# Optimization experiments

Hardware: AMD Instinct MI355X
Metric: run time of the kernel (lower is better)

The kernel has to match this reference:

```python
import jax, jax.numpy as jnp
import numpy as np

N_NODES = 100000
N_EDGES = 1600000
D_IN = 16
D_HID = 32   # 2 * out_channels
D_OUT = 16


def gcn_conv(h, src, dst, W, b, num_nodes):
    """PyG-style GCNConv: x' = D^{-1/2} (A+I) D^{-1/2} (x W) + b.
    src/dst already include self-loops."""
    h = h @ W                                   # [N, F_out] linear transform first
    deg = jnp.zeros((num_nodes,), h.dtype).at[dst].add(1.0)
    dinv = jax.lax.rsqrt(jnp.maximum(deg, 1.0))  # deg >= 1 due to self-loops
    norm = dinv[src] * dinv[dst]                # [E+N]
    msg = h[src] * norm[:, None]                # edge gather (memory-bound)
    out = jax.ops.segment_sum(msg, dst, num_segments=num_nodes)
    return out + b


def setup_inputs() -> dict:
    key = jax.random.key(0)
    k1, k2, k3, k4 = jax.random.split(key, 4)
    x = jnp.arange(N_NODES, dtype=jnp.int32)
    edge_index = jax.random.randint(k1, (2, N_EDGES), 0, N_NODES, dtype=jnp.int32)
    emb = jax.random.normal(k2, (N_NODES, D_IN), dtype=jnp.float32)
    W1 = jax.random.normal(k3, (D_IN, D_HID), dtype=jnp.float32) * (1.0 / np.sqrt(D_IN))
    b1 = jnp.zeros((D_HID,), jnp.float32)
    W2 = jax.random.normal(k4, (D_HID, D_OUT), dtype=jnp.float32) * (1.0 / np.sqrt(D_HID))
    b2 = jnp.zeros((D_OUT,), jnp.float32)
    return {"x": x, "edge_index": edge_index, "emb": emb,
            "W1": W1, "b1": b1, "W2": W2, "b2": b2}


def reference(x, edge_index, emb, W1, b1, W2, b2):
    num_nodes = emb.shape[0]
    # add self-loops once; reused by both conv layers
    loops = jnp.arange(num_nodes, dtype=edge_index.dtype)
    src = jnp.concatenate([edge_index[0], loops])
    dst = jnp.concatenate([edge_index[1], loops])

    h = emb[x]                                  # embedding lookup
    h = jax.nn.relu(gcn_conv(h, src, dst, W1, b1, num_nodes))
    # dropout is identity in eval mode (reference baseline)
    out = gcn_conv(h, src, dst, W2, b2, num_nodes)
    return out
```

## Files before the change

kernel.cpp:

```cpp
#include <hip/hip_runtime.h>


#define BS   256
#define BSBIG 1024
#define NBLK 256
#define BINSHIFT 8
#define BIN  256
#define MAXBINS 512
#define BINCAP 4608

union H2 { int i; _Float16 h[2]; };

__global__ __launch_bounds__(BSBIG) void k_hist(
    const int* __restrict__ dst, int E, int NBINS, int* __restrict__ histG) {
    __shared__ int h[MAXBINS];
    int t = threadIdx.x;
    for (int i = t; i < NBINS; i += BSBIG) h[i] = 0;
    __syncthreads();
    int E4 = E >> 2;
    const int4* d4 = (const int4*)dst;
    for (int i = blockIdx.x * BSBIG + t; i < E4; i += NBLK * BSBIG) {
        int4 d = d4[i];
        atomicAdd(&h[d.x >> BINSHIFT], 1);
        atomicAdd(&h[d.y >> BINSHIFT], 1);
        atomicAdd(&h[d.z >> BINSHIFT], 1);
        atomicAdd(&h[d.w >> BINSHIFT], 1);
    }
    if (blockIdx.x == 0 && t < (E & 3))
        atomicAdd(&h[dst[(E4 << 2) + t] >> BINSHIFT], 1);
    __syncthreads();
    for (int i = t; i < NBINS; i += BSBIG) histG[i * NBLK + blockIdx.x] = h[i];
}

__global__ void k_scanA(const int* __restrict__ in, int L,
                        int* __restrict__ partial, int* __restrict__ bsum) {
    __shared__ int s[BS];
    int t = threadIdx.x;
    int i = blockIdx.x * BS + t;
    int v = (i < L) ? in[i] : 0;
    s[t] = v;
    __syncthreads();
    for (int off = 1; off < BS; off <<= 1) {
        int add = (t >= off) ? s[t - off] : 0;
        __syncthreads();
        s[t] += add;
        __syncthreads();
    }
    if (i < L) partial[i] = s[t] - v;
    if (t == BS - 1) bsum[blockIdx.x] = s[BS - 1];
}

__global__ __launch_bounds__(BSBIG) void k_binscatter(
    const int* __restrict__ src, const int* __restrict__ dst,
    int E, int NBINS, int nB, const int* __restrict__ partial,
    const int* __restrict__ bsum, int* __restrict__ boff,
    int* __restrict__ packed) {
    __shared__ int cur[MAXBINS];
    __shared__ int bofl[MAXBINS];
    __shared__ int ssc[BS];
    int t = threadIdx.x;
    int PERs = (nB + BS - 1) / BS;
    int loc[4];
    int sbase = t * PERs;
    int ssum = 0;
    if (t < BS) {
        for (int j = 0; j < PERs && j < 4; j++) {
            int idx = sbase + j;
            int v = (idx < nB) ? bsum[idx] : 0;
            loc[j] = ssum;
            ssum += v;
        }
        ssc[t] = ssum;
    }
    __syncthreads();
    for (int off = 1; off < BS; off <<= 1) {
        int add = (t < BS && t >= off) ? ssc[t - off] : 0;
        __syncthreads();
        if (t < BS) ssc[t] += add;
        __syncthreads();
    }
    if (t < BS) {
        int ex = ssc[t] - ssum;
        for (int j = 0; j < PERs && j < 4; j++) {
            int idx = sbase + j;
            if (idx < nB) bofl[idx] = ex + loc[j];
        }
    }
    __syncthreads();
    for (int i = t; i < NBINS; i += BSBIG)
        cur[i] = partial[i * NBLK + blockIdx.x] + bofl[i];
    if (blockIdx.x == 0)
        for (int i = t; i < nB; i += BSBIG) boff[i] = bofl[i];
    __syncthreads();
    int E4 = E >> 2;
    const int4* s4 = (const int4*)src;
    const int4* d4 = (const int4*)dst;
    for (int i = blockIdx.x * BSBIG + t; i < E4; i += NBLK * BSBIG) {
        int4 s = s4[i];
        int4 d = d4[i];
        int p0 = atomicAdd(&cur[d.x >> BINSHIFT], 1);
        packed[p0] = s.x | ((d.x & (BIN - 1)) << 18);
        int p1 = atomicAdd(&cur[d.y >> BINSHIFT], 1);
        packed[p1] = s.y | ((d.y & (BIN - 1)) << 18);
        int p2 = atomicAdd(&cur[d.z >> BINSHIFT], 1);
        packed[p2] = s.z | ((d.z & (BIN - 1)) << 18);
        int p3 = atomicAdd(&cur[d.w >> BINSHIFT], 1);
        packed[p3] = s.w | ((d.w & (BIN - 1)) << 18);
    }
    if (blockIdx.x == 0 && t < (E & 3)) {
        int e = (E4 << 2) + t;
        int d = dst[e];
        int p = atomicAdd(&cur[d >> BINSHIFT], 1);
        packed[p] = src[e] | ((d & (BIN - 1)) << 18);
    }
}

__global__ void k_binsort(const int* __restrict__ packed,
                          const int* __restrict__ partial, const int* __restrict__ boff,
                          int NBINS, int N, int E,
                          const int* __restrict__ x, const float* __restrict__ emb,
                          const float* __restrict__ W1,
                          int* __restrict__ row_start, float* __restrict__ dinv,
                          int* __restrict__ col, _Float16* __restrict__ sig1) {
    __shared__ int buf[BINCAP];
    __shared__ int ldeg[BIN];
    __shared__ int lrs[BIN];
    __shared__ int cur[BIN];
    __shared__ float sW[512];
    int b = blockIdx.x;
    int t = threadIdx.x;
    int node0 = b << BINSHIFT;
    int e0 = partial[b * NBLK] + boff[b];
    int e1 = (b + 1 < NBINS) ? (partial[(b + 1) * NBLK] + boff[b + 1]) : E;
    int cnt = e1 - e0;
    bool fits = (cnt <= BINCAP);
    if (b == 0 && t == 0) row_start[N] = E;
    sW[t] = W1[t];
    sW[t + 256] = W1[t + 256];
    ldeg[t] = 0;
    if (fits)
        for (int i = t; i < cnt; i += BS) buf[i] = packed[e0 + i];
    __syncthreads();
    for (int i = t; i < cnt; i += BS) {
        int v = fits ? buf[i] : packed[e0 + i];
        atomicAdd(&ldeg[((unsigned)v >> 18) & (BIN - 1)], 1);
    }
    __syncthreads();
    lrs[t] = ldeg[t];
    __syncthreads();
    for (int off = 1; off < BIN; off <<= 1) {
        int add = (t >= off) ? lrs[t - off] : 0;
        __syncthreads();
        lrs[t] += add;
        __syncthreads();
    }
    int myDeg = ldeg[t];
    int ex = lrs[t] - myDeg;
    cur[t] = ex;
    int n = node0 + t;
    float di = rsqrtf((float)(myDeg + 1));
    if (n < N) {
        row_start[n] = e0 + ex;
        dinv[n] = di;
    }
    __syncthreads();
    for (int i = t; i < cnt; i += BS) {
        int v = fits ? buf[i] : packed[e0 + i];
        int pos = atomicAdd(&cur[((unsigned)v >> 18) & (BIN - 1)], 1);
        col[e0 + pos] = v & 0x3FFFF;
    }
    if (n < N) {
        const float4* er = (const float4*)(emb + (size_t)x[n] * 16);
        float4 ra = er[0], rb = er[1], rc = er[2], rd = er[3];
        float ev[16] = {ra.x, ra.y, ra.z, ra.w, rb.x, rb.y, rb.z, rb.w,
                        rc.x, rc.y, rc.z, rc.w, rd.x, rd.y, rd.z, rd.w};
        int4* s1o = (int4*)sig1;
        #pragma unroll
        for (int cq = 0; cq < 4; cq++) {
            H2 pk[4];
            #pragma unroll
            for (int dw = 0; dw < 4; dw++) {
                int c = cq * 8 + dw * 2;
                float acc0 = 0.f, acc1 = 0.f;
                #pragma unroll
                for (int k = 0; k < 16; k++) {
                    acc0 += ev[k] * sW[k * 32 + c];
                    acc1 += ev[k] * sW[k * 32 + c + 1];
                }
                pk[dw].h[0] = (_Float16)(acc0 * di);
                pk[dw].h[1] = (_Float16)(acc1 * di);
            }
            int4 pv;
            pv.x = pk[0].i; pv.y = pk[1].i; pv.z = pk[2].i; pv.w = pk[3].i;
            s1o[(size_t)n * 4 + cq] = pv;
        }
    }
}

__global__ __launch_bounds__(BS) void k_agg1mm2(
    const _Float16* __restrict__ sig1, const int* __restrict__ row_start,
    const float* __restrict__ dinv, const int* __restrict__ col,
    const float* __restrict__ b1, const float* __restrict__ W2,
    int N, _Float16* __restrict__ sig2) {
    __shared__ float hbuf[4][4][36];
    int t = threadIdx.x;
    int lane = t & 63;
    int wid = t >> 6;
    int g  = lane >> 4;
    int cd = lane & 15;
    int n = blockIdx.x * 16 + wid * 4 + g;
    int nld = (n < N) ? n : N - 1;
    int rs = row_start[nld];
    int re = row_start[nld + 1];
    int dn = (n < N) ? (re - rs) : 0;
    int dnm1 = (dn > 0) ? dn - 1 : 0;
    int dm = dn;
    dm = max(dm, __shfl_xor(dm, 16));
    dm = max(dm, __shfl_xor(dm, 32));
    float w2c[32];
    #pragma unroll
    for (int k = 0; k < 32; k++) w2c[k] = W2[k * 16 + cd];
    const int* s1i = (const int*)sig1;
    float a0 = 0.f, a1 = 0.f;
    int iters = (dm + 7) >> 3;
    int slot = cd & 7;
    int bidx = lane & 48;
    int colv = 0;
    if (iters > 0) {
        int idx = slot; if (idx > dnm1) idx = dnm1;
        colv = col[rs + idx];
    }
    for (int it = 0; it < iters; it++) {
        int e = it << 3;
        int coln = 0;
        if (it + 1 < iters) {
            int idx = e + 8 + slot; if (idx > dnm1) idx = dnm1;
            coln = col[rs + idx];
        }
        int s0 = __shfl(colv, bidx + 0);
        int s1 = __shfl(colv, bidx + 1);
        int s2 = __shfl(colv, bidx + 2);
        int s3 = __shfl(colv, bidx + 3);
        int s4 = __shfl(colv, bidx + 4);
        int s5 = __shfl(colv, bidx + 5);
        int s6 = __shfl(colv, bidx + 6);
        int s7 = __shfl(colv, bidx + 7);
        int u0 = s1i[s0 * 16 + cd];
        int u1 = s1i[s1 * 16 + cd];
        int u2 = s1i[s2 * 16 + cd];
        int u3 = s1i[s3 * 16 + cd];
        int u4 = s1i[s4 * 16 + cd];
        int u5 = s1i[s5 * 16 + cd];
        int u6 = s1i[s6 * 16 + cd];
        int u7 = s1i[s7 * 16 + cd];
        u0 = (e + 0 < dn) ? u0 : 0;
        u1 = (e + 1 < dn) ? u1 : 0;
        u2 = (e + 2 < dn) ? u2 : 0;
        u3 = (e + 3 < dn) ? u3 : 0;
        u4 = (e + 4 < dn) ? u4 : 0;
        u5 = (e + 5 < dn) ? u5 : 0;
        u6 = (e + 6 < dn) ? u6 : 0;
        u7 = (e + 7 < dn) ? u7 : 0;
        H2 p0, p1, p2, p3;
        p0.i = u0; p1.i = u1; p2.i = u2; p3.i = u3;
        a0 += ((float)p0.h[0] + (float)p1.h[0]) + ((float)p2.h[0] + (float)p3.h[0]);
        a1 += ((float)p0.h[1] + (float)p1.h[1]) + ((float)p2.h[1] + (float)p3.h[1]);
        p0.i = u4; p1.i = u5; p2.i = u6; p3.i = u7;
        a0 += ((float)p0.h[0] + (float)p1.h[0]) + ((float)p2.h[0] + (float)p3.h[0]);
        a1 += ((float)p0.h[1] + (float)p1.h[1]) + ((float)p2.h[1] + (float)p3.h[1]);
        colv = coln;
    }
    {
        H2 p; p.i = s1i[nld * 16 + cd];
        a0 += (float)p.h[0];
        a1 += (float)p.h[1];
    }
    float di = dinv[nld];
    float2 b = ((const float2*)b1)[cd];
    float h0 = fmaxf(a0 * di + b.x, 0.f);
    float h1 = fmaxf(a1 * di + b.y, 0.f);
    float* hb = hbuf[wid][g];
    *(float2*)&hb[2 * cd] = make_float2(h0, h1);
    float a = 0.f;
    #pragma unroll
    for (int k = 0; k < 32; k += 4) {
        float4 hv = *(const float4*)&hb[k];
        a = fmaf(hv.x, w2c[k],     a);
        a = fmaf(hv.y, w2c[k + 1], a);
        a = fmaf(hv.z, w2c[k + 2], a);
        a = fmaf(hv.w, w2c[k + 3], a);
    }
    if (n < N) sig2[(size_t)n * 16 + cd] = (_Float16)(a * di);
}

__global__ __launch_bounds__(BS) void k_agg2(
    const _Float16* __restrict__ sig2, const int* __restrict__ row_start,
    const float* __restrict__ dinv, const int* __restrict__ col,
    const float* __restrict__ b2, int N, float* __restrict__ out) {
    int t = threadIdx.x;
    int lane = t & 63;
    int g  = lane >> 4;
    int e2 = (lane >> 3) & 1;
    int cd = lane & 7;
    int n = blockIdx.x * 16 + (t >> 6) * 4 + g;
    int nld = (n < N) ? n : N - 1;
    int rs = row_start[nld];
    int re = row_start[nld + 1];
    int dn = (n < N) ? (re - rs) : 0;
    int dnm1 = (dn > 0) ? dn - 1 : 0;
    int dm = dn;
    dm = max(dm, __shfl_xor(dm, 16));
    dm = max(dm, __shfl_xor(dm, 32));
    const int* s2i = (const int*)sig2;
    float a0 = 0.f, a1 = 0.f;
    int iters = (dm + 15) >> 4;
    int slot = lane & 15;
    int bidx = lane & 48;
    int colv = 0;
    if (iters > 0) {
        int idx = slot; if (idx > dnm1) idx = dnm1;
        colv = col[rs + idx];
    }
    for (int it = 0; it < iters; it++) {
        int e = it << 4;
        int coln = 0;
        if (it + 1 < iters) {
            int idx = e + 16 + slot; if (idx > dnm1) idx = dnm1;
            coln = col[rs + idx];
        }
        #pragma unroll
        for (int j = 0; j < 8; j++) {
            int sl = 2 * j + e2;
            int sv = __shfl(colv, bidx + sl);
            int u = s2i[sv * 8 + cd];
            u = (e + sl < dn) ? u : 0;
            H2 p; p.i = u;
            a0 += (float)p.h[0];
            a1 += (float)p.h[1];
        }
        colv = coln;
    }
    a0 += __shfl_xor(a0, 8);
    a1 += __shfl_xor(a1, 8);
    {
        H2 p; p.i = s2i[nld * 8 + cd];
        a0 += (float)p.h[0];
        a1 += (float)p.h[1];
    }
    if (n < N && e2 == 0) {
        float di = dinv[nld];
        float2 b = ((const float2*)b2)[cd];
        float2 o;
        o.x = a0 * di + b.x;
        o.y = a1 * di + b.y;
        ((float2*)out)[(size_t)n * 8 + cd] = o;
    }
}

extern "C" void kernel_launch(void* const* d_in, const int* in_sizes, int n_in,
                              void* d_out, int out_size, void* d_ws, size_t ws_size,
                              hipStream_t stream) {
    const int*   x   = (const int*)d_in[0];
    const int*   ei  = (const int*)d_in[1];
    const float* emb = (const float*)d_in[2];
    const float* W1  = (const float*)d_in[3];
    const float* b1  = (const float*)d_in[4];
    const float* W2  = (const float*)d_in[5];
    const float* b2  = (const float*)d_in[6];
    float* out = (float*)d_out;

    const int N = in_sizes[0];
    const int E = in_sizes[1] / 2;
    const int* srcp = ei;
    const int* dstp = ei + E;
    const int NBINS = (N + BIN - 1) >> BINSHIFT;
    const int L = NBINS * NBLK;
    const int nB2 = (L + BS - 1) / BS;

    auto al = [](size_t b) { return (b + 255) & ~size_t(255); };
    char* w = (char*)d_ws;
    auto carve = [&](size_t bytes) {
        void* p = (void*)w;
        w += al(bytes);
        return p;
    };
    int*   row_start = (int*)carve((size_t)(N + 1) * 4);
    float* dinv      = (float*)carve((size_t)N * 4);
    int*   col       = (int*)carve((size_t)(E + 256) * 4);
    int*   histG     = (int*)carve((size_t)L * 4);
    int*   partial   = (int*)carve((size_t)L * 4);
    int*   bsum      = (int*)carve((size_t)nB2 * 4);
    int*   boff      = (int*)carve((size_t)nB2 * 4);
    int*   packed    = (int*)carve((size_t)E * 4);
    _Float16* sig1   = (_Float16*)carve((size_t)N * 32 * 2);
    _Float16* sig2   = (_Float16*)carve((size_t)N * 16 * 2);
    (void)ws_size; (void)n_in; (void)out_size;

    int gL = (L + BS - 1) / BS;
    k_hist<<<NBLK, BSBIG, 0, stream>>>(dstp, E, NBINS, histG);
    k_scanA<<<gL, BS, 0, stream>>>(histG, L, partial, bsum);
    k_binscatter<<<NBLK, BSBIG, 0, stream>>>(srcp, dstp, E, NBINS, nB2, partial,
                                             bsum, boff, packed);
    k_binsort<<<NBINS, BS, 0, stream>>>(packed, partial, boff, NBINS, N, E,
                                        x, emb, W1, row_start, dinv, col, sig1);

    int gA = (N + 15) / 16;
    k_agg1mm2<<<gA, BS, 0, stream>>>(sig1, row_start, dinv, col, b1, W2, N, sig2);
    k_agg2<<<gA, BS, 0, stream>>>(sig2, row_start, dinv, col, b2, N, out);
}
```

Measured before the change: 150.4 us.

## Assign one wavefront per node in both aggregation kernels

Both aggregation kernels change from four nodes per wavefront to one node per wavefront. The 64 lanes split the node's neighbour list across edge slots and combine partial sums with cross-lane xor shuffles. The second-layer matmul in k_agg1mm2 is also split across slots and reduced with shuffles. This removes the divergence caused by padding every node in a wave up to the group's maximum degree and exposes more independent gathers per wave. In exchange it launches four times as many blocks, adds shuffle reductions, and leaves many lanes idle for low-degree nodes (average degree is about 17).

```diff
diff --git a/kernel.cpp b/kernel.cpp
--- a/kernel.cpp
+++ b/kernel.cpp
@@ -202,65 +202,71 @@
     const float* __restrict__ dinv, const int* __restrict__ col,
     const float* __restrict__ b1, const float* __restrict__ W2,
     int N, _Float16* __restrict__ sig2) {
-    __shared__ float hbuf[4][4][36];
+    __shared__ __align__(16) float hbuf[4][32];
     int t = threadIdx.x;
     int lane = t & 63;
     int wid = t >> 6;
-    int g  = lane >> 4;
+    int slot = lane >> 4;
     int cd = lane & 15;
-    int n = blockIdx.x * 16 + wid * 4 + g;
+    int n = blockIdx.x * 4 + wid;
     int nld = (n < N) ? n : N - 1;
     int rs = row_start[nld];
     int re = row_start[nld + 1];
     int dn = (n < N) ? (re - rs) : 0;
     int dnm1 = (dn > 0) ? dn - 1 : 0;
-    int dm = dn;
-    dm = max(dm, __shfl_xor(dm, 16));
-    dm = max(dm, __shfl_xor(dm, 32));
-    float w2c[32];
+    float w2c[8];
     #pragma unroll
-    for (int k = 0; k < 32; k++) w2c[k] = W2[k * 16 + cd];
+    for (int j = 0; j < 8; j++) w2c[j] = W2[(slot * 8 + j) * 16 + cd];
     const int* s1i = (const int*)sig1;
     float a0 = 0.f, a1 = 0.f;
-    int iters = (dm + 7) >> 3;
-    int slot = cd & 7;
-    int bidx = lane & 48;
+    int iters = (dn + 7) >> 3;
+    int l31 = lane & 31;
     int colv = 0;
     if (iters > 0) {
-        int idx = slot; if (idx > dnm1) idx = dnm1;
+        int idx = (l31 > dnm1) ? dnm1 : l31;
         colv = col[rs + idx];
     }
-    for (int it = 0; it < iters; it++) {
-        int e = it << 3;
+    for (int g4 = 0; g4 < iters; g4 += 4) {
         int coln = 0;
-        if (it + 1 < iters) {
-            int idx = e + 8 + slot; if (idx > dnm1) idx = dnm1;
+        if (g4 + 4 < iters) {
+            int idx = ((g4 + 4) << 3) + l31;
+            if (idx > dnm1) idx = dnm1;
             coln = col[rs + idx];
         }
-        int s0 = __shfl(colv, bidx + 0);
-        int s1 = __shfl(colv, bidx + 1);
-        int s2 = __shfl(colv, bidx + 2);
-        int s3 = __shfl(colv, bidx + 3);
-        int s4 = __shfl(colv, bidx + 4);
-        int s5 = __shfl(colv, bidx + 5);
-        int s6 = __shfl(colv, bidx + 6);
-        int s7 = __shfl(colv, bidx + 7);
-        int u0 = s1i[s0 * 16 + cd];
-        int u1 = s1i[s1 * 16 + cd];
-        int u2 = s1i[s2 * 16 + cd];
-        int u3 = s1i[s3 * 16 + cd];
-        int u4 = s1i[s4 * 16 + cd];
-        int u5 = s1i[s5 * 16 + cd];
-        int u6 = s1i[s6 * 16 + cd];
-        int u7 = s1i[s7 * 16 + cd];
-        u0 = (e + 0 < dn) ? u0 : 0;
-        u1 = (e + 1 < dn) ? u1 : 0;
-        u2 = (e + 2 < dn) ? u2 : 0;
-        u3 = (e + 3 < dn) ? u3 : 0;
-        u4 = (e + 4 < dn) ? u4 : 0;
-        u5 = (e + 5 < dn) ? u5 : 0;
-        u6 = (e + 6 < dn) ? u6 : 0;
-        u7 = (e + 7 < dn) ? u7 : 0;
+        int u0 = 0, u1 = 0, u2 = 0, u3 = 0, u4 = 0, u5 = 0, u6 = 0, u7 = 0;
+        {
+            int ca = __shfl(colv, slot);
+            int cb = __shfl(colv, slot + 4);
+            u0 = s1i[ca * 16 + cd];
+            u1 = s1i[cb * 16 + cd];
+        }
+        if (g4 + 1 < iters) {
+            int ca = __shfl(colv, 8 + slot);
+            int cb = __shfl(colv, 12 + slot);
+            u2 = s1i[ca * 16 + cd];
+            u3 = s1i[cb * 16 + cd];
+        }
+        if (g4 + 2 < iters) {
+            int ca = __shfl(colv, 16 + slot);
+            int cb = __shfl(colv, 20 + slot);
+            u4 = s1i[ca * 16 + cd];
+            u5 = s1i[cb * 16 + cd];
+        }
+        if (g4 + 3 < iters) {
+            int ca = __shfl(colv, 24 + slot);
+            int cb = __shfl(colv, 28 + slot);
+            u6 = s1i[ca * 16 + cd];
+            u7 = s1i[cb * 16 + cd];
+        }
+        int e = g4 << 3;
+        u0 = (e + slot      < dn) ? u0 : 0;
+        u1 = (e + slot + 4  < dn) ? u1 : 0;
+        u2 = (e + slot + 8  < dn) ? u2 : 0;
+        u3 = (e + slot + 12 < dn) ? u3 : 0;
+        u4 = (e + slot + 16 < dn) ? u4 : 0;
+        u5 = (e + slot + 20 < dn) ? u5 : 0;
+        u6 = (e + slot + 24 < dn) ? u6 : 0;
+        u7 = (e + slot + 28 < dn) ? u7 : 0;
         H2 p0, p1, p2, p3;
         p0.i = u0; p1.i = u1; p2.i = u2; p3.i = u3;
         a0 += ((float)p0.h[0] + (float)p1.h[0]) + ((float)p2.h[0] + (float)p3.h[0]);
@@ -270,6 +276,8 @@
         a1 += ((float)p0.h[1] + (float)p1.h[1]) + ((float)p2.h[1] + (float)p3.h[1]);
         colv = coln;
     }
+    a0 += __shfl_xor(a0, 16); a1 += __shfl_xor(a1, 16);
+    a0 += __shfl_xor(a0, 32); a1 += __shfl_xor(a1, 32);
     {
         H2 p; p.i = s1i[nld * 16 + cd];
         a0 += (float)p.h[0];
@@ -279,18 +287,15 @@
     float2 b = ((const float2*)b1)[cd];
     float h0 = fmaxf(a0 * di + b.x, 0.f);
     float h1 = fmaxf(a1 * di + b.y, 0.f);
-    float* hb = hbuf[wid][g];
-    *(float2*)&hb[2 * cd] = make_float2(h0, h1);
-    float a = 0.f;
-    #pragma unroll
-    for (int k = 0; k < 32; k += 4) {
-        float4 hv = *(const float4*)&hb[k];
-        a = fmaf(hv.x, w2c[k],     a);
-        a = fmaf(hv.y, w2c[k + 1], a);
-        a = fmaf(hv.z, w2c[k + 2], a);
-        a = fmaf(hv.w, w2c[k + 3], a);
-    }
-    if (n < N) sig2[(size_t)n * 16 + cd] = (_Float16)(a * di);
+    float* hb = hbuf[wid];
+    if (slot == 0) *(float2*)&hb[2 * cd] = make_float2(h0, h1);
+    float4 hv0 = *(const float4*)&hb[slot * 8];
+    float4 hv1 = *(const float4*)&hb[slot * 8 + 4];
+    float a = hv0.x * w2c[0] + hv0.y * w2c[1] + hv0.z * w2c[2] + hv0.w * w2c[3]
+            + hv1.x * w2c[4] + hv1.y * w2c[5] + hv1.z * w2c[6] + hv1.w * w2c[7];
+    a += __shfl_xor(a, 16);
+    a += __shfl_xor(a, 32);
+    if (n < N && lane < 16) sig2[(size_t)n * 16 + cd] = (_Float16)(a * di);
 }
 
 __global__ __launch_bounds__(BS) void k_agg2(
@@ -299,55 +304,58 @@
     const float* __restrict__ b2, int N, float* __restrict__ out) {
     int t = threadIdx.x;
     int lane = t & 63;
-    int g  = lane >> 4;
-    int e2 = (lane >> 3) & 1;
+    int slot = lane >> 3;
     int cd = lane & 7;
-    int n = blockIdx.x * 16 + (t >> 6) * 4 + g;
+    int n = blockIdx.x * 4 + (t >> 6);
     int nld = (n < N) ? n : N - 1;
     int rs = row_start[nld];
     int re = row_start[nld + 1];
     int dn = (n < N) ? (re - rs) : 0;
     int dnm1 = (dn > 0) ? dn - 1 : 0;
-    int dm = dn;
-    dm = max(dm, __shfl_xor(dm, 16));
-    dm = max(dm, __shfl_xor(dm, 32));
     const int* s2i = (const int*)sig2;
     float a0 = 0.f, a1 = 0.f;
-    int iters = (dm + 15) >> 4;
-    int slot = lane & 15;
-    int bidx = lane & 48;
+    int iters = (dn + 7) >> 3;
+    int l31 = lane & 31;
     int colv = 0;
     if (iters > 0) {
-        int idx = slot; if (idx > dnm1) idx = dnm1;
+        int idx = (l31 > dnm1) ? dnm1 : l31;
         colv = col[rs + idx];
     }
-    for (int it = 0; it < iters; it++) {
-        int e = it << 4;
+    for (int g4 = 0; g4 < iters; g4 += 4) {
         int coln = 0;
-        if (it + 1 < iters) {
-            int idx = e + 16 + slot; if (idx > dnm1) idx = dnm1;
+        if (g4 + 4 < iters) {
+            int idx = ((g4 + 4) << 3) + l31;
+            if (idx > dnm1) idx = dnm1;
             coln = col[rs + idx];
         }
-        #pragma unroll
-        for (int j = 0; j < 8; j++) {
-            int sl = 2 * j + e2;
-            int sv = __shfl(colv, bidx + sl);
-            int u = s2i[sv * 8 + cd];
-            u = (e + sl < dn) ? u : 0;
-            H2 p; p.i = u;
-            a0 += (float)p.h[0];
-            a1 += (float)p.h[1];
-        }
+        int u0 = 0, u1 = 0, u2 = 0, u3 = 0;
+        {
+            int c0 = __shfl(colv, slot);
+            u0 = s2i[c0 * 8 + cd];
+        }
+        if (g4 + 1 < iters) { int c1 = __shfl(colv, 8 + slot);  u1 = s2i[c1 * 8 + cd]; }
+        if (g4 + 2 < iters) { int c2 = __shfl(colv, 16 + slot); u2 = s2i[c2 * 8 + cd]; }
+        if (g4 + 3 < iters) { int c3 = __shfl(colv, 24 + slot); u3 = s2i[c3 * 8 + cd]; }
+        int e = g4 << 3;
+        u0 = (e + slot      < dn) ? u0 : 0;
+        u1 = (e + slot + 8  < dn) ? u1 : 0;
+        u2 = (e + slot + 16 < dn) ? u2 : 0;
+        u3 = (e + slot + 24 < dn) ? u3 : 0;
+        H2 p0, p1, p2, p3;
+        p0.i = u0; p1.i = u1; p2.i = u2; p3.i = u3;
+        a0 += ((float)p0.h[0] + (float)p1.h[0]) + ((float)p2.h[0] + (float)p3.h[0]);
+        a1 += ((float)p0.h[1] + (float)p1.h[1]) + ((float)p2.h[1] + (float)p3.h[1]);
         colv = coln;
     }
-    a0 += __shfl_xor(a0, 8);
-    a1 += __shfl_xor(a1, 8);
+    a0 += __shfl_xor(a0, 8);  a1 += __shfl_xor(a1, 8);
+    a0 += __shfl_xor(a0, 16); a1 += __shfl_xor(a1, 16);
+    a0 += __shfl_xor(a0, 32); a1 += __shfl_xor(a1, 32);
     {
         H2 p; p.i = s2i[nld * 8 + cd];
         a0 += (float)p.h[0];
         a1 += (float)p.h[1];
     }
-    if (n < N && e2 == 0) {
+    if (n < N && slot == 0) {
         float di = dinv[nld];
         float2 b = ((const float2*)b2)[cd];
         float2 o;
@@ -404,7 +412,7 @@
     k_binsort<<<NBINS, BS, 0, stream>>>(packed, partial, boff, NBINS, N, E,
                                         x, emb, W1, row_start, dinv, col, sig1);
 
-    int gA = (N + 15) / 16;
+    int gA = (N + 3) / 4;
     k_agg1mm2<<<gA, BS, 0, stream>>>(sig1, row_start, dinv, col, b1, W2, N, sig2);
     k_agg2<<<gA, BS, 0, stream>>>(sig2, row_start, dinv, col, b2, N, out);
 }
```

Result: slower. 180.0 us (+19.7%).

## Fuse histogram and bin scatter using atomic per-bin slot reservation

Applied to the files above, without the earlier changes.

Merges the histogram, global scan and bin-scatter kernels into one kernel. Each block reserves space in a fixed-stride per-bin region with one global atomicAdd per bin, and the per-bin offsets are recomputed by a small scan inside k_binsort. This removes two kernel launches and the histogram/partial-sum round trips through global memory. In exchange it needs a memset, and the fixed per-bin capacity (4608) can overflow into the next bin on skewed degree distributions. Edge order within a bin also becomes nondeterministic.

```diff
diff --git a/kernel.cpp b/kernel.cpp
--- a/kernel.cpp
+++ b/kernel.cpp
@@ -8,17 +8,21 @@
 #define BIN  256
 #define MAXBINS 512
 #define BINCAP 4608
+#define BINSTRIDE 4608
 
 union H2 { int i; _Float16 h[2]; };
 
-__global__ __launch_bounds__(BSBIG) void k_hist(
-    const int* __restrict__ dst, int E, int NBINS, int* __restrict__ histG) {
+__global__ __launch_bounds__(BSBIG) void k_scatter(
+    const int* __restrict__ src, const int* __restrict__ dst,
+    int E, int NBINS, int* __restrict__ gbin, int* __restrict__ packed) {
     __shared__ int h[MAXBINS];
+    __shared__ int cur[MAXBINS];
     int t = threadIdx.x;
     for (int i = t; i < NBINS; i += BSBIG) h[i] = 0;
     __syncthreads();
     int E4 = E >> 2;
     const int4* d4 = (const int4*)dst;
+    const int4* s4 = (const int4*)src;
     for (int i = blockIdx.x * BSBIG + t; i < E4; i += NBLK * BSBIG) {
         int4 d = d4[i];
         atomicAdd(&h[d.x >> BINSHIFT], 1);
@@ -29,72 +33,9 @@
     if (blockIdx.x == 0 && t < (E & 3))
         atomicAdd(&h[dst[(E4 << 2) + t] >> BINSHIFT], 1);
     __syncthreads();
-    for (int i = t; i < NBINS; i += BSBIG) histG[i * NBLK + blockIdx.x] = h[i];
-}
-
-__global__ void k_scanA(const int* __restrict__ in, int L,
-                        int* __restrict__ partial, int* __restrict__ bsum) {
-    __shared__ int s[BS];
-    int t = threadIdx.x;
-    int i = blockIdx.x * BS + t;
-    int v = (i < L) ? in[i] : 0;
-    s[t] = v;
-    __syncthreads();
-    for (int off = 1; off < BS; off <<= 1) {
-        int add = (t >= off) ? s[t - off] : 0;
-        __syncthreads();
-        s[t] += add;
-        __syncthreads();
-    }
-    if (i < L) partial[i] = s[t] - v;
-    if (t == BS - 1) bsum[blockIdx.x] = s[BS - 1];
-}
-
-__global__ __launch_bounds__(BSBIG) void k_binscatter(
-    const int* __restrict__ src, const int* __restrict__ dst,
-    int E, int NBINS, int nB, const int* __restrict__ partial,
-    const int* __restrict__ bsum, int* __restrict__ boff,
-    int* __restrict__ packed) {
-    __shared__ int cur[MAXBINS];
-    __shared__ int bofl[MAXBINS];
-    __shared__ int ssc[BS];
-    int t = threadIdx.x;
-    int PERs = (nB + BS - 1) / BS;
-    int loc[4];
-    int sbase = t * PERs;
-    int ssum = 0;
-    if (t < BS) {
-        for (int j = 0; j < PERs && j < 4; j++) {
-            int idx = sbase + j;
-            int v = (idx < nB) ? bsum[idx] : 0;
-            loc[j] = ssum;
-            ssum += v;
-        }
-        ssc[t] = ssum;
-    }
-    __syncthreads();
-    for (int off = 1; off < BS; off <<= 1) {
-        int add = (t < BS && t >= off) ? ssc[t - off] : 0;
-        __syncthreads();
-        if (t < BS) ssc[t] += add;
-        __syncthreads();
-    }
-    if (t < BS) {
-        int ex = ssc[t] - ssum;
-        for (int j = 0; j < PERs && j < 4; j++) {
-            int idx = sbase + j;
-            if (idx < nB) bofl[idx] = ex + loc[j];
-        }
-    }
-    __syncthreads();
     for (int i = t; i < NBINS; i += BSBIG)
-        cur[i] = partial[i * NBLK + blockIdx.x] + bofl[i];
-    if (blockIdx.x == 0)
-        for (int i = t; i < nB; i += BSBIG) boff[i] = bofl[i];
-    __syncthreads();
-    int E4 = E >> 2;
-    const int4* s4 = (const int4*)src;
-    const int4* d4 = (const int4*)dst;
+        cur[i] = i * BINSTRIDE + atomicAdd(&gbin[i], h[i]);
+    __syncthreads();
     for (int i = blockIdx.x * BSBIG + t; i < E4; i += NBLK * BSBIG) {
         int4 s = s4[i];
         int4 d = d4[i];
@@ -116,7 +57,7 @@
 }
 
 __global__ void k_binsort(const int* __restrict__ packed,
-                          const int* __restrict__ partial, const int* __restrict__ boff,
+                          const int* __restrict__ gbin,
                           int NBINS, int N, int E,
                           const int* __restrict__ x, const float* __restrict__ emb,
                           const float* __restrict__ W1,
@@ -126,23 +67,51 @@
     __shared__ int ldeg[BIN];
     __shared__ int lrs[BIN];
     __shared__ int cur[BIN];
+    __shared__ int ssc[BS];
+    __shared__ int bofl[MAXBINS];
     __shared__ float sW[512];
     int b = blockIdx.x;
     int t = threadIdx.x;
     int node0 = b << BINSHIFT;
-    int e0 = partial[b * NBLK] + boff[b];
-    int e1 = (b + 1 < NBINS) ? (partial[(b + 1) * NBLK] + boff[b + 1]) : E;
-    int cnt = e1 - e0;
+    int PERs = (NBINS + BS - 1) / BS;
+    int loc[4];
+    int sbase = t * PERs;
+    int ssum = 0;
+    for (int j = 0; j < PERs && j < 4; j++) {
+        int idx = sbase + j;
+        int v = (idx < NBINS) ? gbin[idx] : 0;
+        loc[j] = ssum;
+        ssum += v;
+    }
+    ssc[t] = ssum;
+    __syncthreads();
+    for (int off = 1; off < BS; off <<= 1) {
+        int add = (t >= off) ? ssc[t - off] : 0;
+        __syncthreads();
+        ssc[t] += add;
+        __syncthreads();
+    }
+    {
+        int ex = ssc[t] - ssum;
+        for (int j = 0; j < PERs && j < 4; j++) {
+            int idx = sbase + j;
+            if (idx < NBINS) bofl[idx] = ex + loc[j];
+        }
+    }
+    __syncthreads();
+    int e0 = bofl[b];
+    int cnt = gbin[b];
+    int p0 = b * BINSTRIDE;
     bool fits = (cnt <= BINCAP);
     if (b == 0 && t == 0) row_start[N] = E;
     sW[t] = W1[t];
     sW[t + 256] = W1[t + 256];
     ldeg[t] = 0;
     if (fits)
-        for (int i = t; i < cnt; i += BS) buf[i] = packed[e0 + i];
+        for (int i = t; i < cnt; i += BS) buf[i] = packed[p0 + i];
     __syncthreads();
     for (int i = t; i < cnt; i += BS) {
-        int v = fits ? buf[i] : packed[e0 + i];
+        int v = fits ? buf[i] : packed[p0 + i];
         atomicAdd(&ldeg[((unsigned)v >> 18) & (BIN - 1)], 1);
     }
     __syncthreads();
@@ -165,7 +134,7 @@
     }
     __syncthreads();
     for (int i = t; i < cnt; i += BS) {
-        int v = fits ? buf[i] : packed[e0 + i];
+        int v = fits ? buf[i] : packed[p0 + i];
         int pos = atomicAdd(&cur[((unsigned)v >> 18) & (BIN - 1)], 1);
         col[e0 + pos] = v & 0x3FFFF;
     }
@@ -374,8 +343,6 @@
     const int* srcp = ei;
     const int* dstp = ei + E;
     const int NBINS = (N + BIN - 1) >> BINSHIFT;
-    const int L = NBINS * NBLK;
-    const int nB2 = (L + BS - 1) / BS;
 
     auto al = [](size_t b) { return (b + 255) & ~size_t(255); };
     char* w = (char*)d_ws;
@@ -387,21 +354,15 @@
     int*   row_start = (int*)carve((size_t)(N + 1) * 4);
     float* dinv      = (float*)carve((size_t)N * 4);
     int*   col       = (int*)carve((size_t)(E + 256) * 4);
-    int*   histG     = (int*)carve((size_t)L * 4);
-    int*   partial   = (int*)carve((size_t)L * 4);
-    int*   bsum      = (int*)carve((size_t)nB2 * 4);
-    int*   boff      = (int*)carve((size_t)nB2 * 4);
-    int*   packed    = (int*)carve((size_t)E * 4);
+    int*   gbin      = (int*)carve((size_t)NBINS * 4);
+    int*   packed    = (int*)carve((size_t)NBINS * BINSTRIDE * 4);
     _Float16* sig1   = (_Float16*)carve((size_t)N * 32 * 2);
     _Float16* sig2   = (_Float16*)carve((size_t)N * 16 * 2);
     (void)ws_size; (void)n_in; (void)out_size;
 
-    int gL = (L + BS - 1) / BS;
-    k_hist<<<NBLK, BSBIG, 0, stream>>>(dstp, E, NBINS, histG);
-    k_scanA<<<gL, BS, 0, stream>>>(histG, L, partial, bsum);
-    k_binscatter<<<NBLK, BSBIG, 0, stream>>>(srcp, dstp, E, NBINS, nB2, partial,
-                                             bsum, boff, packed);
-    k_binsort<<<NBINS, BS, 0, stream>>>(packed, partial, boff, NBINS, N, E,
+    hipMemsetAsync(gbin, 0, (size_t)NBINS * 4, stream);
+    k_scatter<<<NBLK, BSBIG, 0, stream>>>(srcp, dstp, E, NBINS, gbin, packed);
+    k_binsort<<<NBINS, BS, 0, stream>>>(packed, gbin, NBINS, N, E,
                                         x, emb, W1, row_start, dinv, col, sig1);
 
     int gA = (N + 15) / 16;
```

Measured after the change: 150.5 us. No clear change (+0.0%).
